# Optimization experiments

Measured on AMD Instinct MI355X. Metric: run time of the kernel, lower is better.

Reference implementation:

```python
import jax, jax.numpy as jnp
import numpy as np

NUM_PROPOSALS = 200000
NUM_OBJECTS = 128
N_CLS = 256
POS_THR = 0.4
NEG_THR = 0.1
REG_FACTOR = 10.0


def _make_boxes(key, n, img=1000.0, max_wh=200.0):
    k1, k2 = jax.random.split(key)
    xy = jax.random.uniform(k1, (n, 2), jnp.float32) * (img - max_wh)
    wh = jax.random.uniform(k2, (n, 2), jnp.float32) * (max_wh - 1.0) + 1.0
    return jnp.concatenate([xy, xy + wh], axis=-1)  # valid xyxy boxes


def setup_inputs() -> dict:
    key = jax.random.key(0)
    k1, k2, k3 = jax.random.split(key, 3)
    return {
        "objectness_score": jax.random.normal(k1, (NUM_PROPOSALS,), jnp.float32),
        "proposals": _make_boxes(k2, NUM_PROPOSALS),
        "gt_bounding_box": _make_boxes(k3, NUM_OBJECTS)[None],  # (1, N, 4)
    }


def _box_iou(b1, b2):
    # b1: (N,4), b2: (M,4) in xyxy -> (N, M)
    a1 = (b1[:, 2] - b1[:, 0]) * (b1[:, 3] - b1[:, 1])
    a2 = (b2[:, 2] - b2[:, 0]) * (b2[:, 3] - b2[:, 1])
    lt = jnp.maximum(b1[:, None, :2], b2[None, :, :2])
    rb = jnp.minimum(b1[:, None, 2:], b2[None, :, 2:])
    wh = jnp.clip(rb - lt, 0.0)
    inter = wh[..., 0] * wh[..., 1]
    return inter / (a1[:, None] + a2[None, :] - inter)


def _rpn_loss(objectness_score, proposals, gt_bounding_box):
    gt = gt_bounding_box[0]                      # (N, 4)
    iou = _box_iou(gt, proposals)                # (N, M)
    N, M = iou.shape
    flat = iou.reshape(-1)                       # (N*M,)

    # top-N best (gt, proposal) pairs, indices only (non-differentiable path)
    _, best_idx = jax.lax.top_k(flat, N)

    key = jax.random.key(42)
    k1, k2, k3 = jax.random.split(key, 3)
    neg_inf = jnp.float32(-jnp.inf)

    # random-priority sampling == randperm + truncate over candidate multiset
    pos_prio = jnp.where(flat > POS_THR, jax.random.uniform(k1, (N * M,)), neg_inf)
    best_prio = jax.random.uniform(k2, (N,))
    cand_prio = jnp.concatenate([best_prio, pos_prio])
    cand_idx = jnp.concatenate([best_idx, jnp.arange(N * M)])

    num_pos = N_CLS // 2   # always filled: best_idx contributes N=128 candidates
    num_neg = N_CLS - num_pos

    sel_p, loc = jax.lax.top_k(cand_prio, num_pos)
    pos_flat = cand_idx[loc]
    pos_valid = jnp.isfinite(sel_p)
    pos_rows = pos_flat // M
    pos_cols = pos_flat % M

    neg_prio = jnp.where(flat < NEG_THR, jax.random.uniform(k3, (N * M,)), neg_inf)
    sel_n, neg_flat = jax.lax.top_k(neg_prio, num_neg)
    neg_valid = jnp.isfinite(sel_n)
    neg_cols = neg_flat % M

    # classification: BCE-with-logits, mean over valid samples
    logits = jnp.concatenate([objectness_score[pos_cols], objectness_score[neg_cols]])
    labels = jnp.concatenate([jnp.ones((num_pos,), jnp.float32), jnp.zeros((num_neg,), jnp.float32)])
    w = jnp.concatenate([pos_valid, neg_valid]).astype(jnp.float32)
    bce = jnp.maximum(logits, 0.0) - logits * labels + jnp.log1p(jnp.exp(-jnp.abs(logits)))
    cls_loss = jnp.sum(bce * w) / jnp.maximum(jnp.sum(w), 1.0)

    d = proposals[pos_cols] - gt[pos_rows]       # (num_pos, 4)
    ad = jnp.abs(d)
    sl1 = jnp.where(ad < 1.0, 0.5 * d * d, ad - 0.5)
    wp = pos_valid.astype(jnp.float32)[:, None]
    reg_loss = jnp.sum(sl1 * wp) / jnp.maximum(jnp.sum(wp) * 4.0, 1.0)

    return cls_loss + REG_FACTOR * reg_loss


def reference(objectness_score, proposals, gt_bounding_box):
    return _rpn_loss(objectness_score, proposals, gt_bounding_box)
```

## Files before the change

### kernel.cpp

```cpp
#include <hip/hip_runtime.h>
#include <stdint.h>

#pragma clang fp contract(off)

typedef unsigned long long u64;
typedef uint32_t u32;

#define M_PROP 200000u
#define N_GT   128u
#define NM     25600000u
#define GSPLIT 4u
#define GPART  32u

#define BCUT 8355840u
#define CCUT 8387584u
#define IB_POS 0x3ECCCCCDu

#define SHARDS 16u
#define SHARD_CAP 4096u
#define ACAP_SHARD 65536u
#define TOPA_CAP 8192u
#define COMP_CAP 8192u
#define ACAP_L 512u

#define CSLOT(i) counters[(u32)(i) * 256u]

__device__ inline u32 rotl32(u32 x, u32 r) { return __builtin_rotateleft32(x, r); }

__device__ inline u32 lane_prefix(u64 mask) {
  return __builtin_amdgcn_mbcnt_hi((u32)(mask >> 32),
                                   __builtin_amdgcn_mbcnt_lo((u32)mask, 0u));
}

__host__ __device__ inline void tf2x32(u32 k0, u32 k1, u32 x0, u32 x1,
                                       u32& o0, u32& o1) {
  u32 ks0 = k0, ks1 = k1, ks2 = k0 ^ k1 ^ 0x1BD11BDAu;
  x0 += ks0; x1 += ks1;
#ifdef __HIP_DEVICE_COMPILE__
#define TF_R(r) { x0 += x1; x1 = rotl32(x1, r); x1 ^= x0; }
#else
#define TF_R(r) { x0 += x1; x1 = (x1 << r) | (x1 >> (32 - r)); x1 ^= x0; }
#endif
  TF_R(13) TF_R(15) TF_R(26) TF_R(6)
  x0 += ks1; x1 += ks2 + 1u;
  TF_R(17) TF_R(29) TF_R(16) TF_R(24)
  x0 += ks2; x1 += ks0 + 2u;
  TF_R(13) TF_R(15) TF_R(26) TF_R(6)
  x0 += ks0; x1 += ks1 + 3u;
  TF_R(17) TF_R(29) TF_R(16) TF_R(24)
  x0 += ks1; x1 += ks2 + 4u;
  TF_R(13) TF_R(15) TF_R(26) TF_R(6)
  x0 += ks2; x1 += ks0 + 5u;
#undef TF_R
  o0 = x0; o1 = x1;
}

__device__ inline u32 jax_bits32(u32 ka, u32 kb, u32 idx) {
  u32 a, b; tf2x32(ka, kb, 0u, idx, a, b);
  return a ^ b;
}

static void jax_split3(u32& k1a, u32& k1b, u32& k2a, u32& k2b,
                       u32& k3a, u32& k3b) {
  const u32 K0 = 0u, K1 = 42u;
  tf2x32(K0, K1, 0u, 0u, k1a, k1b);
  tf2x32(K0, K1, 0u, 1u, k2a, k2b);
  tf2x32(K0, K1, 0u, 2u, k3a, k3b);
}

__device__ inline u32 wave_append_slot(u32* ctr, bool pred, bool& any) {
  u64 mask = __ballot(pred);
  if (mask == 0ull) { any = false; return 0u; }
  any = true;
  u32 prefix = lane_prefix(mask);
  int leader = __ffsll(mask) - 1;
  u32 base = 0u;
  if ((int)(threadIdx.x & 63u) == leader)
    base = atomicAdd(ctr, (u32)__popcll(mask));
  base = __shfl(base, leader, 64);
  return base + prefix;
}

__device__ inline void wave_append4(u32* ctr, u64* buf, u32 cap,
                                    const bool* p, const u64* v) {
  u64 m0 = __ballot(p[0]);
  u64 m1 = __ballot(p[1]);
  u64 m2 = __ballot(p[2]);
  u64 m3 = __ballot(p[3]);
  u32 n0 = (u32)__popcll(m0), n1 = (u32)__popcll(m1);
  u32 n2 = (u32)__popcll(m2), n3 = (u32)__popcll(m3);
  int leader = __ffsll(m0 | m1 | m2 | m3) - 1;
  u32 base = 0u;
  if ((int)(threadIdx.x & 63u) == leader)
    base = atomicAdd(ctr, n0 + n1 + n2 + n3);
  base = __shfl(base, leader, 64);
  if (p[0]) { u32 s = base + lane_prefix(m0); if (s < cap) buf[s] = v[0]; }
  base += n0;
  if (p[1]) { u32 s = base + lane_prefix(m1); if (s < cap) buf[s] = v[1]; }
  base += n1;
  if (p[2]) { u32 s = base + lane_prefix(m2); if (s < cap) buf[s] = v[2]; }
  base += n2;
  if (p[3]) { u32 s = base + lane_prefix(m3); if (s < cap) buf[s] = v[3]; }
}

__device__ inline u32 iouBin(u32 bits) {
  u32 b = (bits - 0x3E800000u) >> 14;
  return b > 1023u ? 1023u : b;
}

__global__ __launch_bounds__(256) void rpn_collect(
    const float4* __restrict__ props, const float4* __restrict__ gt,
    u64* __restrict__ bufA, u64* __restrict__ bufB, u64* __restrict__ bufC,
    u32* __restrict__ counters, u32* __restrict__ gHistA,
    u32 k1a, u32 k1b, u32 k3a, u32 k3b) {
  __shared__ float4 gtS[GPART];
  __shared__ float gtAreaS[GPART];
  __shared__ u32 hA[1024];
  __shared__ u32 listA[4][ACAP_L];
  const u32 tid = threadIdx.x;
  const u32 lane = tid & 63u;
  const u32 wid = tid >> 6;
  const u32 gbase = blockIdx.y * GPART;
  for (u32 i = tid; i < 1024u; i += 256u) hA[i] = 0u;
  for (u32 j = tid; j < GPART; j += 256u) {
    float4 gb = gt[gbase + j];
    gtS[j] = gb;
    gtAreaS[j] = (gb.z - gb.x) * (gb.w - gb.y);
  }
  __syncthreads();

  const u32 shard = (blockIdx.x * GSPLIT + blockIdx.y) & (SHARDS - 1u);
  u32* cntC_g = &CSLOT(shard);
  u32* cntB_g = &CSLOT(16u + shard);
  u32* cntA_g = &CSLOT(32u + shard);
  u64* myBufC = bufC + (size_t)shard * SHARD_CAP;
  u64* myBufB = bufB + (size_t)shard * SHARD_CAP;
  u64* myBufA = bufA + (size_t)shard * ACAP_SHARD;

  u32 p = blockIdx.x * 256u + tid;
  bool active = p < M_PROP;
  float4 pb = make_float4(0.f, 0.f, 0.f, 0.f);
  if (active) pb = props[p];
  float pa = (pb.z - pb.x) * (pb.w - pb.y);

  u32 cntA = 0u;

#define PROCESS_A()                                                          \
  {                                                                          \
    for (u32 i = lane; i < cntA; i += 64u) {                                 \
      u32 aidx = listA[wid][i];                                              \
      u32 row = aidx / M_PROP;                                               \
      u32 col = aidx - row * M_PROP;                                         \
      float4 pbx = props[col];                                               \
      float4 gbx = gtS[row - gbase];                                         \
      float gax = gtAreaS[row - gbase];                                      \
      float pax = (pbx.z - pbx.x) * (pbx.w - pbx.y);                         \
      float wxx = fminf(gbx.z, pbx.z) - fmaxf(gbx.x, pbx.x);                 \
      float wyy = fminf(gbx.w, pbx.w) - fmaxf(gbx.y, pbx.y);                 \
      wxx = fmaxf(wxx, 0.0f); wyy = fmaxf(wyy, 0.0f);                        \
      float interx = wxx * wyy;                                              \
      float ioux = interx / (gax + pax - interx);                            \
      u32 ib = __float_as_uint(ioux);                                        \
      bool isA = ioux > 0.25f;                                               \
      if (isA) atomicAdd(&hA[iouBin(ib)], 1u);                               \
      bool anyk;                                                             \
      u32 sk = wave_append_slot(cntA_g, isA, anyk);                          \
      if (isA && sk < ACAP_SHARD)                                            \
        myBufA[sk] = ((u64)ib << 25) | (u64)(0x1FFFFFFu - aidx);             \
      u32 m1 = jax_bits32(k1a, k1b, aidx) >> 9;                              \
      bool keep = isA && (ib > IB_POS) && (m1 >= BCUT);                      \
      bool anyb;                                                             \
      u32 sb2 = wave_append_slot(cntB_g, keep, anyb);                        \
      if (keep && sb2 < SHARD_CAP)                                           \
        myBufB[sb2] = ((u64)m1 << 25) | (u64)(0x1FFFFFFu - (aidx + 128u));   \
    }                                                                        \
    cntA = 0u;                                                               \
  }

  u32 idxRun = gbase * M_PROP + p;
  for (u32 gg = 0u; gg < GPART; gg += 4u) {
    float inter[4], uni[4]; u32 idx[4], m3[4];
    bool aa[4], ccp[4];
#pragma unroll
    for (u32 r = 0u; r < 4u; ++r) {
      float4 gb = gtS[gg + r];
      float ga = gtAreaS[gg + r];
      float wx = fminf(gb.z, pb.z) - fmaxf(gb.x, pb.x);
      float wy = fminf(gb.w, pb.w) - fmaxf(gb.y, pb.y);
      wx = fmaxf(wx, 0.0f); wy = fmaxf(wy, 0.0f);
      inter[r] = wx * wy;
      uni[r] = ga + pa - inter[r];
      idx[r] = idxRun; idxRun += M_PROP;
      m3[r] = jax_bits32(k3a, k3b, idx[r]) >> 9;
      aa[r] = active && (inter[r] > 0.2499f * uni[r]);
      ccp[r] = active && (m3[r] >= CCUT);
    }
#pragma unroll
    for (u32 r = 0u; r < 4u; ++r) {
      u64 ma = __ballot(aa[r]);
      if (ma) {
        u32 pfx = lane_prefix(ma);
        if (aa[r]) listA[wid][cntA + pfx] = idx[r];
        cntA += (u32)__popcll(ma);
      }
    }
    u64 mc = __ballot(ccp[0] | ccp[1] | ccp[2] | ccp[3]);
    if (mc) {
      bool cc[4]; u64 cv[4];
#pragma unroll
      for (u32 r = 0u; r < 4u; ++r) {
        float iouX = inter[r] / uni[r];
        cc[r] = ccp[r] && (iouX < 0.1f);
        cv[r] = ((u64)m3[r] << 25) | (u64)(0x1FFFFFFu - idx[r]);
      }
      wave_append4(cntC_g, myBufC, SHARD_CAP, cc, cv);
    }
    if (cntA > ACAP_L - 256u) PROCESS_A();
  }
  PROCESS_A();
#undef PROCESS_A

  __syncthreads();
  for (u32 b = tid; b < 1024u; b += 256u) {
    u32 v = hA[b];
    if (v) atomicAdd(&gHistA[b], v);
  }
}

__global__ __launch_bounds__(256) void rpn_filterA(
    const u64* __restrict__ bufA, const u32* __restrict__ gHistA,
    u32* __restrict__ counters, u64* __restrict__ bufTopA) {
  const u32 tid = threadIdx.x;
  const u32 lane = tid & 63u;
  u32 loc[16]; u32 t = 0u;
  const u32 bbase = lane * 16u;
#pragma unroll
  for (u32 j = 0u; j < 16u; ++j) { loc[j] = gHistA[bbase + j]; t += loc[j]; }
  u32 suf = t;
  for (u32 off = 1u; off < 64u; off <<= 1u) {
    u32 o = __shfl_down(suf, off, 64);
    if (lane + off < 64u) suf += o;
  }
  u32 cum = suf - t;
  u32 cand = 0u; bool found = false;
#pragma unroll
  for (int j = 15; j >= 0; --j) {
    cum += loc[j];
    if (!found && cum >= 128u) { cand = bbase + (u32)j; found = true; }
  }
  for (u32 off = 1u; off < 64u; off <<= 1u) {
    u32 o = __shfl_xor(cand, off, 64);
    cand = o > cand ? o : cand;
  }
  const u32 cut = cand;
  for (u32 sh = 0u; sh < SHARDS; ++sh) {
    u32 n = CSLOT(32u + sh); n = n < ACAP_SHARD ? n : ACAP_SHARD;
    const u64* sb = bufA + (size_t)sh * ACAP_SHARD;
    for (u32 i = blockIdx.x * 256u + tid; i < n; i += gridDim.x * 256u) {
      u64 k = sb[i];
      bool keep = iouBin((u32)(k >> 25)) >= cut;
      bool any;
      u32 s = wave_append_slot(&CSLOT(48), keep, any);
      if (keep && s < TOPA_CAP) bufTopA[s] = k;
    }
  }
}

__device__ inline void rank_select(const u64* cand, u32 nc, u64* selKey) {
  const u32 tid = threadIdx.x;
  if (tid < 128u) selKey[tid] = 0ull;
  u64 k[8]; u32 r[8];
#pragma unroll
  for (int j = 0; j < 8; ++j) {
    u32 i = tid + (u32)j * 1024u;
    k[j] = (i < nc) ? cand[i] : 0ull;
    r[j] = 0u;
  }
  __syncthreads();
  for (u32 i = 0u; i < nc; ++i) {
    u64 v = cand[i];
#pragma unroll
    for (int j = 0; j < 8; ++j) r[j] += (v > k[j]) ? 1u : 0u;
  }
#pragma unroll
  for (int j = 0; j < 8; ++j) {
    u32 i = tid + (u32)j * 1024u;
    if (i < nc && r[j] < 128u) selKey[r[j]] = k[j];
  }
  __syncthreads();
}

__device__ inline void rank_select2(const u64* cand, u32 nc, u64* selKey) {
  const u32 tid = threadIdx.x;
  if (tid < 128u) selKey[tid] = 0ull;
  u64 mine = (tid < nc) ? cand[tid] : 0ull;
  __syncthreads();
  u32 r = 0u;
  for (u32 i = 0u; i < nc; ++i) r += (cand[i] > mine) ? 1u : 0u;
  if (tid < nc && r < 128u) selKey[r] = mine;
  __syncthreads();
}

__device__ inline float sl1(float d) {
  float ad = fabsf(d);
  return (ad < 1.0f) ? 0.5f * d * d : ad - 0.5f;
}

__global__ __launch_bounds__(1024) void rpn_finalize(
    const float* __restrict__ obj, const float4* __restrict__ props,
    const float4* __restrict__ gt,
    const u64* __restrict__ bufTopA,
    const u64* __restrict__ bufB, const u64* __restrict__ bufC,
    const u32* __restrict__ counters, float* __restrict__ out,
    u32 k2a, u32 k2b) {
  __shared__ u64 keyBuf[COMP_CAP];
  __shared__ u64 keyBuf2[1024];
  __shared__ u64 selKey[128];
  __shared__ u32 bestIdx[128];
  __shared__ u32 hist64[64];
  __shared__ float pr[16];
  __shared__ u32 s_cnt, s_cnt2, s_cutLo;
  __shared__ float s_reg, s_bcep;

  const u32 tid = threadIdx.x;
  const u32 lane = tid & 63u;
  const u32 wid = tid >> 6u;

  u32 nT = CSLOT(48); nT = nT < TOPA_CAP ? nT : TOPA_CAP;
  for (u32 i = tid; i < nT; i += 1024u) keyBuf[i] = bufTopA[i];
  __syncthreads();
  if (nT <= 1024u) rank_select2(keyBuf, nT, selKey);
  else rank_select(keyBuf, nT, selKey);
  if (tid < 128u) {
    u64 k = selKey[tid];
    bestIdx[tid] = (k == 0ull) ? 0u : (0x1FFFFFFu - (u32)(k & 0x1FFFFFFu));
  }
  __syncthreads();

  if (tid == 0u) { s_cnt = 128u; s_cnt2 = 0u; }
  if (tid < 64u) hist64[tid] = 0u;
  __syncthreads();
  if (tid < 128u) {
    u32 m2 = jax_bits32(k2a, k2b, tid) >> 9;
    keyBuf[tid] = ((u64)m2 << 25) | (u64)(0x1FFFFFFu - tid);
    if (m2 >= BCUT) atomicAdd(&hist64[(m2 - BCUT) >> 9], 1u);
  }
  {
    u32 n = CSLOT(16u + wid); n = n < SHARD_CAP ? n : SHARD_CAP;
    const u64* sb = bufB + (size_t)wid * SHARD_CAP;
    for (u32 i = lane; i < n; i += 64u) {
      u64 k = sb[i];
      bool any;
      u32 s = wave_append_slot(&s_cnt, true, any);
      if (s < COMP_CAP) keyBuf[s] = k;
      atomicAdd(&hist64[((u32)(k >> 25) - BCUT) >> 9], 1u);
    }
  }
  __syncthreads();
  u32 nc = s_cnt < COMP_CAP ? s_cnt : COMP_CAP;
  if (wid == 0u) {
    u32 suf = hist64[lane];
    for (u32 off = 1u; off < 64u; off <<= 1u) {
      u32 o = __shfl_down(suf, off, 64);
      if (lane + off < 64u) suf += o;
    }
    u64 ok = __ballot(suf >= 128u);
    u32 cutLo = 0u;
    if (ok) cutLo = BCUT + ((63u - (u32)__clzll(ok)) << 9);
    if (lane == 0u) s_cutLo = cutLo;
  }
  __syncthreads();
  {
    u64 cutKey = ((u64)s_cutLo) << 25;
    for (u32 i = tid; i < nc; i += 1024u) {
      u64 k = keyBuf[i];
      if (k >= cutKey) {
        u32 s = atomicAdd(&s_cnt2, 1u);
        if (s < 1024u) keyBuf2[s] = k;
      }
    }
  }
  __syncthreads();
  u32 ns = s_cnt2;
  if (ns <= 1024u) rank_select2(keyBuf2, ns, selKey);
  else rank_select(keyBuf, nc, selKey);

  float locReg = 0.0f, locBce = 0.0f;
  if (tid < 128u) {
    u64 k = selKey[tid];
    if (k != 0ull) {
      u32 c = 0x1FFFFFFu - (u32)(k & 0x1FFFFFFu);
      u32 pair = (c < 128u) ? bestIdx[c] : (c - 128u);
      if (pair < NM) {
        u32 row = pair / M_PROP, col = pair % M_PROP;
        float4 prb = props[col];
        float4 gb = gt[row];
        locReg = sl1(prb.x - gb.x) + sl1(prb.y - gb.y) +
                 sl1(prb.z - gb.z) + sl1(prb.w - gb.w);
        float l = obj[col];
        locBce = fmaxf(l, 0.0f) - l + log1pf(expf(-fabsf(l)));
      }
    }
  }
  {
    float v = locReg;
    for (u32 off = 32u; off > 0u; off >>= 1u) v += __shfl_xor(v, off, 64);
    if (lane == 0u) pr[wid] = v;
    __syncthreads();
    if (tid == 0u) {
      float s = 0.0f;
#pragma unroll
      for (u32 w = 0u; w < 16u; ++w) s += pr[w];
      s_reg = s;
    }
    __syncthreads();
    v = locBce;
    for (u32 off = 32u; off > 0u; off >>= 1u) v += __shfl_xor(v, off, 64);
    if (lane == 0u) pr[wid] = v;
    __syncthreads();
    if (tid == 0u) {
      float s = 0.0f;
#pragma unroll
      for (u32 w = 0u; w < 16u; ++w) s += pr[w];
      s_bcep = s;
    }
    __syncthreads();
  }

  if (tid == 0u) { s_cnt = 0u; s_cnt2 = 0u; }
  if (tid < 64u) hist64[tid] = 0u;
  __syncthreads();
  {
    u32 n = CSLOT(wid); n = n < SHARD_CAP ? n : SHARD_CAP;
    const u64* sb = bufC + (size_t)wid * SHARD_CAP;
    for (u32 i = lane; i < n; i += 64u) {
      u64 k = sb[i];
      bool any;
      u32 s = wave_append_slot(&s_cnt, true, any);
      if (s < COMP_CAP) keyBuf[s] = k;
      atomicAdd(&hist64[((u32)(k >> 25) - CCUT) >> 4], 1u);
    }
  }
  __syncthreads();
  nc = s_cnt < COMP_CAP ? s_cnt : COMP_CAP;
  if (wid == 0u) {
    u32 suf = hist64[lane];
    for (u32 off = 1u; off < 64u; off <<= 1u) {
      u32 o = __shfl_down(suf, off, 64);
      if (lane + off < 64u) suf += o;
    }
    u64 ok = __ballot(suf >= 128u);
    u32 cutLo = 0u;
    if (ok) cutLo = CCUT + ((63u - (u32)__clzll(ok)) << 4);
    if (lane == 0u) s_cutLo = cutLo;
  }
  __syncthreads();
  {
    u64 cutKey = ((u64)s_cutLo) << 25;
    for (u32 i = tid; i < nc; i += 1024u) {
      u64 k = keyBuf[i];
      if (k >= cutKey) {
        u32 s = atomicAdd(&s_cnt2, 1u);
        if (s < 1024u) keyBuf2[s] = k;
      }
    }
  }
  __syncthreads();
  ns = s_cnt2;
  if (ns <= 1024u) rank_select2(keyBuf2, ns, selKey);
  else rank_select(keyBuf, nc, selKey);

  float locBceN = 0.0f;
  if (tid < 128u) {
    u64 k = selKey[tid];
    if (k != 0ull) {
      u32 idx = 0x1FFFFFFu - (u32)(k & 0x1FFFFFFu);
      u32 col = idx % M_PROP;
      float l = obj[col];
      locBceN = fmaxf(l, 0.0f) + log1pf(expf(-fabsf(l)));
    }
  }
  {
    float v = locBceN;
    for (u32 off = 32u; off > 0u; off >>= 1u) v += __shfl_xor(v, off, 64);
    if (lane == 0u) pr[wid] = v;
    __syncthreads();
    if (tid == 0u) {
      float s = 0.0f;
#pragma unroll
      for (u32 w = 0u; w < 16u; ++w) s += pr[w];
      float cls = (s_bcep + s) / 256.0f;
      float reg = s_reg / 512.0f;
      out[0] = cls + 10.0f * reg;
    }
  }
}

extern "C" void kernel_launch(void* const* d_in, const int* in_sizes, int n_in,
                              void* d_out, int out_size, void* d_ws, size_t ws_size,
                              hipStream_t stream) {
  (void)in_sizes; (void)n_in; (void)out_size; (void)ws_size;
  const float* obj = (const float*)d_in[0];
  const float4* props = (const float4*)d_in[1];
  const float4* gt = (const float4*)d_in[2];
  float* out = (float*)d_out;

  u32 k1a, k1b, k2a, k2b, k3a, k3b;
  jax_split3(k1a, k1b, k2a, k2b, k3a, k3b);

  uint8_t* base = (uint8_t*)d_ws;
  u32* counters = (u32*)base;
  u32* gHistA = (u32*)(base + 65536);
  u64* bufTopA = (u64*)(base + 65536 + 4096);
  u64* bufB = (u64*)(base + 65536 + 4096 + (size_t)TOPA_CAP * 8);
  u64* bufC = bufB + (size_t)SHARDS * SHARD_CAP;
  u64* bufA = bufC + (size_t)SHARDS * SHARD_CAP;

  const u32 gridX = (M_PROP + 255u) / 256u;
  hipMemsetAsync(d_ws, 0, 65536 + 4096, stream);
  rpn_collect<<<dim3(gridX, GSPLIT), 256, 0, stream>>>(
      props, gt, bufA, bufB, bufC, counters, gHistA, k1a, k1b, k3a, k3b);
  rpn_filterA<<<64, 256, 0, stream>>>(bufA, gHistA, counters, bufTopA);
  rpn_finalize<<<1, 1024, 0, stream>>>(obj, props, gt, bufTopA, bufB, bufC,
                                       counters, out, k2a, k2b);
}
```

Before: 107.9 us.

## Split collect kernel into separate IoU-candidate and negative-sampling block groups

The collect grid is now split into two kinds of blocks. Two y-slices handle 64 GT rows each and do only the IoU-based positive and high-IoU list work. Four y-slices handle 32 rows each and do the negative sampling: they compute the threefry bits first and compute IoU only when some lane in the wave passes the random cut. This separates the divergent workloads and skips IoU divisions for most negative candidates. The change also shrinks the counter stride and memset size, and reshapes filterA to 256 blocks with one shard per block, at the cost of duplicated proposal loads and more blocks overall.

```diff
diff --git a/kernel.cpp b/kernel.cpp
--- a/kernel.cpp
+++ b/kernel.cpp
@@ -9,8 +9,8 @@
 #define M_PROP 200000u
 #define N_GT   128u
 #define NM     25600000u
-#define GSPLIT 4u
-#define GPART  32u
+#define ASPLIT 2u
+#define CSPLIT 4u
 
 #define BCUT 8355840u
 #define CCUT 8387584u
@@ -21,9 +21,9 @@
 #define ACAP_SHARD 65536u
 #define TOPA_CAP 8192u
 #define COMP_CAP 8192u
-#define ACAP_L 512u
-
-#define CSLOT(i) counters[(u32)(i) * 256u]
+#define ALIST 512u
+
+#define CSLOT(i) counters[(u32)(i) * 64u]
 
 __device__ inline u32 rotl32(u32 x, u32 r) { return __builtin_rotateleft32(x, r); }
 
@@ -81,28 +81,6 @@
   return base + prefix;
 }
 
-__device__ inline void wave_append4(u32* ctr, u64* buf, u32 cap,
-                                    const bool* p, const u64* v) {
-  u64 m0 = __ballot(p[0]);
-  u64 m1 = __ballot(p[1]);
-  u64 m2 = __ballot(p[2]);
-  u64 m3 = __ballot(p[3]);
-  u32 n0 = (u32)__popcll(m0), n1 = (u32)__popcll(m1);
-  u32 n2 = (u32)__popcll(m2), n3 = (u32)__popcll(m3);
-  int leader = __ffsll(m0 | m1 | m2 | m3) - 1;
-  u32 base = 0u;
-  if ((int)(threadIdx.x & 63u) == leader)
-    base = atomicAdd(ctr, n0 + n1 + n2 + n3);
-  base = __shfl(base, leader, 64);
-  if (p[0]) { u32 s = base + lane_prefix(m0); if (s < cap) buf[s] = v[0]; }
-  base += n0;
-  if (p[1]) { u32 s = base + lane_prefix(m1); if (s < cap) buf[s] = v[1]; }
-  base += n1;
-  if (p[2]) { u32 s = base + lane_prefix(m2); if (s < cap) buf[s] = v[2]; }
-  base += n2;
-  if (p[3]) { u32 s = base + lane_prefix(m3); if (s < cap) buf[s] = v[3]; }
-}
-
 __device__ inline u32 iouBin(u32 bits) {
   u32 b = (bits - 0x3E800000u) >> 14;
   return b > 1023u ? 1023u : b;
@@ -113,117 +91,147 @@
     u64* __restrict__ bufA, u64* __restrict__ bufB, u64* __restrict__ bufC,
     u32* __restrict__ counters, u32* __restrict__ gHistA,
     u32 k1a, u32 k1b, u32 k3a, u32 k3b) {
-  __shared__ float4 gtS[GPART];
-  __shared__ float gtAreaS[GPART];
+  __shared__ float4 gtS[64];
+  __shared__ float gtAreaS[64];
   __shared__ u32 hA[1024];
-  __shared__ u32 listA[4][ACAP_L];
+  __shared__ u32 listA[4][ALIST];
   const u32 tid = threadIdx.x;
   const u32 lane = tid & 63u;
   const u32 wid = tid >> 6;
-  const u32 gbase = blockIdx.y * GPART;
-  for (u32 i = tid; i < 1024u; i += 256u) hA[i] = 0u;
-  for (u32 j = tid; j < GPART; j += 256u) {
-    float4 gb = gt[gbase + j];
-    gtS[j] = gb;
-    gtAreaS[j] = (gb.z - gb.x) * (gb.w - gb.y);
-  }
-  __syncthreads();
-
-  const u32 shard = (blockIdx.x * GSPLIT + blockIdx.y) & (SHARDS - 1u);
-  u32* cntC_g = &CSLOT(shard);
-  u32* cntB_g = &CSLOT(16u + shard);
-  u32* cntA_g = &CSLOT(32u + shard);
-  u64* myBufC = bufC + (size_t)shard * SHARD_CAP;
-  u64* myBufB = bufB + (size_t)shard * SHARD_CAP;
-  u64* myBufA = bufA + (size_t)shard * ACAP_SHARD;
-
+  const u32 y = blockIdx.y;
   u32 p = blockIdx.x * 256u + tid;
   bool active = p < M_PROP;
-  float4 pb = make_float4(0.f, 0.f, 0.f, 0.f);
-  if (active) pb = props[p];
-  float pa = (pb.z - pb.x) * (pb.w - pb.y);
-
-  u32 cntA = 0u;
+
+  if (y < ASPLIT) {
+    const u32 gbase = y * 64u;
+    for (u32 i = tid; i < 1024u; i += 256u) hA[i] = 0u;
+    for (u32 j = tid; j < 64u; j += 256u) {
+      float4 gb = gt[gbase + j];
+      gtS[j] = gb;
+      gtAreaS[j] = (gb.z - gb.x) * (gb.w - gb.y);
+    }
+    __syncthreads();
+    const u32 shard = (blockIdx.x * ASPLIT + y) & (SHARDS - 1u);
+    u32* cntB_g = &CSLOT(16u + shard);
+    u32* cntA_g = &CSLOT(32u + shard);
+    u64* myBufB = bufB + (size_t)shard * SHARD_CAP;
+    u64* myBufA = bufA + (size_t)shard * ACAP_SHARD;
+
+    float4 pb = make_float4(0.f, 0.f, 0.f, 0.f);
+    if (active) pb = props[p];
+    float pa = (pb.z - pb.x) * (pb.w - pb.y);
+    u32 cntA = 0u;
 
 #define PROCESS_A()                                                          \
-  {                                                                          \
-    for (u32 i = lane; i < cntA; i += 64u) {                                 \
-      u32 aidx = listA[wid][i];                                              \
-      u32 row = aidx / M_PROP;                                               \
-      u32 col = aidx - row * M_PROP;                                         \
-      float4 pbx = props[col];                                               \
-      float4 gbx = gtS[row - gbase];                                         \
-      float gax = gtAreaS[row - gbase];                                      \
-      float pax = (pbx.z - pbx.x) * (pbx.w - pbx.y);                         \
-      float wxx = fminf(gbx.z, pbx.z) - fmaxf(gbx.x, pbx.x);                 \
-      float wyy = fminf(gbx.w, pbx.w) - fmaxf(gbx.y, pbx.y);                 \
-      wxx = fmaxf(wxx, 0.0f); wyy = fmaxf(wyy, 0.0f);                        \
-      float interx = wxx * wyy;                                              \
-      float ioux = interx / (gax + pax - interx);                            \
-      u32 ib = __float_as_uint(ioux);                                        \
-      bool isA = ioux > 0.25f;                                               \
-      if (isA) atomicAdd(&hA[iouBin(ib)], 1u);                               \
-      bool anyk;                                                             \
-      u32 sk = wave_append_slot(cntA_g, isA, anyk);                          \
-      if (isA && sk < ACAP_SHARD)                                            \
-        myBufA[sk] = ((u64)ib << 25) | (u64)(0x1FFFFFFu - aidx);             \
-      u32 m1 = jax_bits32(k1a, k1b, aidx) >> 9;                              \
-      bool keep = isA && (ib > IB_POS) && (m1 >= BCUT);                      \
-      bool anyb;                                                             \
-      u32 sb2 = wave_append_slot(cntB_g, keep, anyb);                        \
-      if (keep && sb2 < SHARD_CAP)                                           \
-        myBufB[sb2] = ((u64)m1 << 25) | (u64)(0x1FFFFFFu - (aidx + 128u));   \
-    }                                                                        \
-    cntA = 0u;                                                               \
-  }
-
-  u32 idxRun = gbase * M_PROP + p;
-  for (u32 gg = 0u; gg < GPART; gg += 4u) {
-    float inter[4], uni[4]; u32 idx[4], m3[4];
-    bool aa[4], ccp[4];
-#pragma unroll
-    for (u32 r = 0u; r < 4u; ++r) {
-      float4 gb = gtS[gg + r];
-      float ga = gtAreaS[gg + r];
-      float wx = fminf(gb.z, pb.z) - fmaxf(gb.x, pb.x);
-      float wy = fminf(gb.w, pb.w) - fmaxf(gb.y, pb.y);
-      wx = fmaxf(wx, 0.0f); wy = fmaxf(wy, 0.0f);
-      inter[r] = wx * wy;
-      uni[r] = ga + pa - inter[r];
-      idx[r] = idxRun; idxRun += M_PROP;
-      m3[r] = jax_bits32(k3a, k3b, idx[r]) >> 9;
-      aa[r] = active && (inter[r] > 0.2499f * uni[r]);
-      ccp[r] = active && (m3[r] >= CCUT);
-    }
-#pragma unroll
-    for (u32 r = 0u; r < 4u; ++r) {
-      u64 ma = __ballot(aa[r]);
-      if (ma) {
-        u32 pfx = lane_prefix(ma);
-        if (aa[r]) listA[wid][cntA + pfx] = idx[r];
-        cntA += (u32)__popcll(ma);
-      }
-    }
-    u64 mc = __ballot(ccp[0] | ccp[1] | ccp[2] | ccp[3]);
-    if (mc) {
-      bool cc[4]; u64 cv[4];
+    {                                                                        \
+      for (u32 i = lane; i < cntA; i += 64u) {                               \
+        u32 aidx = listA[wid][i];                                            \
+        u32 row = aidx / M_PROP;                                             \
+        u32 col = aidx - row * M_PROP;                                       \
+        float4 pbx = props[col];                                             \
+        float4 gbx = gtS[row - gbase];                                       \
+        float gax = gtAreaS[row - gbase];                                    \
+        float pax = (pbx.z - pbx.x) * (pbx.w - pbx.y);                       \
+        float wxx = fminf(gbx.z, pbx.z) - fmaxf(gbx.x, pbx.x);               \
+        float wyy = fminf(gbx.w, pbx.w) - fmaxf(gbx.y, pbx.y);               \
+        wxx = fmaxf(wxx, 0.0f); wyy = fmaxf(wyy, 0.0f);                      \
+        float interx = wxx * wyy;                                            \
+        float ioux = interx / (gax + pax - interx);                          \
+        u32 ib = __float_as_uint(ioux);                                      \
+        bool isA = ioux > 0.25f;                                             \
+        if (isA) atomicAdd(&hA[iouBin(ib)], 1u);                             \
+        bool anyk;                                                           \
+        u32 sk = wave_append_slot(cntA_g, isA, anyk);                        \
+        if (isA && sk < ACAP_SHARD)                                          \
+          myBufA[sk] = ((u64)ib << 25) | (u64)(0x1FFFFFFu - aidx);           \
+        u32 m1 = jax_bits32(k1a, k1b, aidx) >> 9;                            \
+        bool keep = isA && (ib > IB_POS) && (m1 >= BCUT);                    \
+        bool anyb;                                                           \
+        u32 sb2 = wave_append_slot(cntB_g, keep, anyb);                      \
+        if (keep && sb2 < SHARD_CAP)                                         \
+          myBufB[sb2] = ((u64)m1 << 25) | (u64)(0x1FFFFFFu - (aidx + 128u)); \
+      }                                                                      \
+      cntA = 0u;                                                             \
+    }
+
+    for (u32 gg = 0u; gg < 64u; gg += 4u) {
+      bool aa[4];
 #pragma unroll
       for (u32 r = 0u; r < 4u; ++r) {
-        float iouX = inter[r] / uni[r];
-        cc[r] = ccp[r] && (iouX < 0.1f);
-        cv[r] = ((u64)m3[r] << 25) | (u64)(0x1FFFFFFu - idx[r]);
-      }
-      wave_append4(cntC_g, myBufC, SHARD_CAP, cc, cv);
-    }
-    if (cntA > ACAP_L - 256u) PROCESS_A();
-  }
-  PROCESS_A();
+        float4 gb = gtS[gg + r];
+        float ga = gtAreaS[gg + r];
+        float wx = fminf(gb.z, pb.z) - fmaxf(gb.x, pb.x);
+        float wy = fminf(gb.w, pb.w) - fmaxf(gb.y, pb.y);
+        wx = fmaxf(wx, 0.0f); wy = fmaxf(wy, 0.0f);
+        float inter = wx * wy;
+        float uni = ga + pa - inter;
+        aa[r] = active && (inter > 0.2499f * uni);
+      }
+#pragma unroll
+      for (u32 r = 0u; r < 4u; ++r) {
+        u64 ma = __ballot(aa[r]);
+        if (ma) {
+          u32 pfx = lane_prefix(ma);
+          if (aa[r]) listA[wid][cntA + pfx] = (gbase + gg + r) * M_PROP + p;
+          cntA += (u32)__popcll(ma);
+        }
+      }
+      if (cntA > ALIST - 256u) PROCESS_A();
+    }
+    PROCESS_A();
 #undef PROCESS_A
 
-  __syncthreads();
-  for (u32 b = tid; b < 1024u; b += 256u) {
-    u32 v = hA[b];
-    if (v) atomicAdd(&gHistA[b], v);
+    __syncthreads();
+    for (u32 b = tid; b < 1024u; b += 256u) {
+      u32 v = hA[b];
+      if (v) atomicAdd(&gHistA[b], v);
+    }
+  } else {
+    const u32 gbase = (y - ASPLIT) * 32u;
+    for (u32 j = tid; j < 32u; j += 256u) {
+      float4 gb = gt[gbase + j];
+      gtS[j] = gb;
+      gtAreaS[j] = (gb.z - gb.x) * (gb.w - gb.y);
+    }
+    __syncthreads();
+    const u32 shard = (blockIdx.x * CSPLIT + (y - ASPLIT)) & (SHARDS - 1u);
+    u32* cntC_g = &CSLOT(shard);
+    u64* myBufC = bufC + (size_t)shard * SHARD_CAP;
+
+    u32 idxR = gbase * M_PROP + p;
+    for (u32 gg = 0u; gg < 32u; gg += 8u) {
+      u32 m3v[8], idxv[8];
+      bool pre[8];
+#pragma unroll
+      for (u32 r = 0u; r < 8u; ++r) {
+        idxv[r] = idxR; idxR += M_PROP;
+        m3v[r] = jax_bits32(k3a, k3b, idxv[r]) >> 9;
+        pre[r] = m3v[r] >= CCUT;
+      }
+      bool anyp = pre[0] | pre[1] | pre[2] | pre[3] |
+                  pre[4] | pre[5] | pre[6] | pre[7];
+      u64 mp = __ballot(anyp);
+      if (mp) {
+        float4 pbx = make_float4(0.f, 0.f, 0.f, 0.f);
+        if (active) pbx = props[p];
+        float pax = (pbx.z - pbx.x) * (pbx.w - pbx.y);
+#pragma unroll
+        for (u32 r = 0u; r < 8u; ++r) {
+          float4 gb = gtS[gg + r];
+          float ga = gtAreaS[gg + r];
+          float wx = fminf(gb.z, pbx.z) - fmaxf(gb.x, pbx.x);
+          float wy = fminf(gb.w, pbx.w) - fmaxf(gb.y, pbx.y);
+          wx = fmaxf(wx, 0.0f); wy = fmaxf(wy, 0.0f);
+          float inter = wx * wy;
+          float iouX = inter / (ga + pax - inter);
+          bool cc = active && pre[r] && (iouX < 0.1f);
+          bool any;
+          u32 s = wave_append_slot(cntC_g, cc, any);
+          if (cc && s < SHARD_CAP)
+            myBufC[s] = ((u64)m3v[r] << 25) | (u64)(0x1FFFFFFu - idxv[r]);
+        }
+      }
+    }
   }
 }
 
@@ -253,16 +261,16 @@
     cand = o > cand ? o : cand;
   }
   const u32 cut = cand;
-  for (u32 sh = 0u; sh < SHARDS; ++sh) {
-    u32 n = CSLOT(32u + sh); n = n < ACAP_SHARD ? n : ACAP_SHARD;
-    const u64* sb = bufA + (size_t)sh * ACAP_SHARD;
-    for (u32 i = blockIdx.x * 256u + tid; i < n; i += gridDim.x * 256u) {
-      u64 k = sb[i];
-      bool keep = iouBin((u32)(k >> 25)) >= cut;
-      bool any;
-      u32 s = wave_append_slot(&CSLOT(48), keep, any);
-      if (keep && s < TOPA_CAP) bufTopA[s] = k;
-    }
+  const u32 sh = blockIdx.x & (SHARDS - 1u);
+  const u32 chunk = blockIdx.x >> 4;
+  u32 n = CSLOT(32u + sh); n = n < ACAP_SHARD ? n : ACAP_SHARD;
+  const u64* sb = bufA + (size_t)sh * ACAP_SHARD;
+  for (u32 i = chunk * 256u + tid; i < n; i += 16u * 256u) {
+    u64 k = sb[i];
+    bool keep = iouBin((u32)(k >> 25)) >= cut;
+    bool any;
+    u32 s = wave_append_slot(&CSLOT(48), keep, any);
+    if (keep && s < TOPA_CAP) bufTopA[s] = k;
   }
 }
 
@@ -510,17 +518,17 @@
 
   uint8_t* base = (uint8_t*)d_ws;
   u32* counters = (u32*)base;
-  u32* gHistA = (u32*)(base + 65536);
-  u64* bufTopA = (u64*)(base + 65536 + 4096);
-  u64* bufB = (u64*)(base + 65536 + 4096 + (size_t)TOPA_CAP * 8);
+  u32* gHistA = (u32*)(base + 16384);
+  u64* bufTopA = (u64*)(base + 16384 + 4096);
+  u64* bufB = (u64*)(base + 16384 + 4096 + (size_t)TOPA_CAP * 8);
   u64* bufC = bufB + (size_t)SHARDS * SHARD_CAP;
   u64* bufA = bufC + (size_t)SHARDS * SHARD_CAP;
 
   const u32 gridX = (M_PROP + 255u) / 256u;
-  hipMemsetAsync(d_ws, 0, 65536 + 4096, stream);
-  rpn_collect<<<dim3(gridX, GSPLIT), 256, 0, stream>>>(
+  hipMemsetAsync(d_ws, 0, 16384 + 4096, stream);
+  rpn_collect<<<dim3(gridX, ASPLIT + CSPLIT), 256, 0, stream>>>(
       props, gt, bufA, bufB, bufC, counters, gHistA, k1a, k1b, k3a, k3b);
-  rpn_filterA<<<64, 256, 0, stream>>>(bufA, gHistA, counters, bufTopA);
+  rpn_filterA<<<256, 256, 0, stream>>>(bufA, gHistA, counters, bufTopA);
   rpn_finalize<<<1, 1024, 0, stream>>>(obj, props, gt, bufTopA, bufB, bufC,
                                        counters, out, k2a, k2b);
 }
```

Result: faster. 102.1 us (-5.3%).
